# Kernel tuning notes

Hardware: AMD Instinct MI355X
Metric: run time of the kernel (lower is better)

## Reference

```python
import jax, jax.numpy as jnp
import numpy as np

NEG_BIG = -9e15  # matches torch's -9000000000000000.0 mask value
ALPHA = 0.2      # LeakyReLU negative slope


def setup_inputs() -> dict:
    key = jax.random.key(0)
    k1, k2, k3 = jax.random.split(key, 3)
    B, N, Fin, Fout = 8, 2048, 64, 64
    h = jax.random.normal(k1, (B, N, Fin), dtype=jnp.float32)
    adj = jax.random.randint(k2, (B, N, N), 0, 2, dtype=jnp.int32)
    kW, ka = jax.random.split(k3)
    # xavier_uniform with gain=1.414
    gW = 1.414 * np.sqrt(6.0 / (Fin + Fout))
    W = jax.random.uniform(kW, (Fin, Fout), minval=-gW, maxval=gW, dtype=jnp.float32)
    ga = 1.414 * np.sqrt(6.0 / (2 * Fout + 1))
    a = jax.random.uniform(ka, (2 * Fout, 1), minval=-ga, maxval=ga, dtype=jnp.float32)
    return {"h": h, "adj": adj, "W": W, "a": a}


def reference(h, adj, W, a):
    # Wh: [B, N, Fout]
    Wh = jnp.einsum("bnf,fo->bno", h, W)
    Fout = W.shape[1]
    a1 = a[:Fout, 0]   # source part of attention vector
    a2 = a[Fout:, 0]   # target part
    # e_ij = leakyrelu(a1.Wh_i + a2.Wh_j) -- rank-1 decomposition of the
    # repeat/cat construction; avoids the [B,N,N,2F] intermediate.
    s = Wh @ a1        # [B, N]
    t = Wh @ a2        # [B, N]
    e = s[:, :, None] + t[:, None, :]            # [B, N, N]
    e = jnp.where(e > 0, e, ALPHA * e)           # LeakyReLU
    e = jnp.where(adj > 0, e, NEG_BIG)           # adjacency mask
    attention = jax.nn.softmax(e, axis=2)
    # dropout omitted: reference is eval-mode (F.dropout is identity when not training)
    h_prime = jnp.einsum("bij,bjo->bio", attention, Wh)
    return jax.nn.elu(h_prime)                   # concat=True branch
```

## Files before the change

### kernel.cpp

```cpp
#include <hip/hip_runtime.h>


#define NB 8
#define NN 2048
#define NF 64
#define ALPHA 0.2f

typedef __attribute__((ext_vector_type(8))) short  short8;
typedef __attribute__((ext_vector_type(4))) float  f32x4;

static __device__ __forceinline__ unsigned short f2bf(float f) {
    unsigned u = __builtin_bit_cast(unsigned, f);
    u += 0x7fffu + ((u >> 16) & 1u);
    return (unsigned short)(u >> 16);
}

__global__ __launch_bounds__(256) void k1_wh_st(
    const float* __restrict__ h, const float* __restrict__ W,
    const float* __restrict__ a, unsigned short* __restrict__ whT,
    float* __restrict__ sw, float* __restrict__ tw)
{
    __shared__ float W_l[64 * 65];
    __shared__ float wa[128];
    __shared__ float tile[4 * 16 * 65];

    const int tid  = threadIdx.x;
    const int lane = tid & 63, wv = tid >> 6;
    const int im   = lane & 15, kq = lane >> 4;

    #pragma unroll
    for (int k = 0; k < 16; ++k) {
        int e = tid + 256 * k;
        W_l[(e >> 6) * 65 + (e & 63)] = W[e];
    }
    __syncthreads();

    if (tid < 128) {
        int f = tid & 63;
        const float* ap = a + (tid >> 6) * 64;
        float acc = 0.f;
        #pragma unroll 8
        for (int o = 0; o < 64; ++o) acc += W_l[f * 65 + o] * ap[o];
        wa[tid] = acc;
    }
    __syncthreads();

    short8 bf[4][2];
    #pragma unroll
    for (int nb = 0; nb < 4; ++nb)
        #pragma unroll
        for (int ks = 0; ks < 2; ++ks)
            #pragma unroll
            for (int u = 0; u < 8; ++u)
                bf[nb][ks][u] = (short)f2bf(W_l[(ks * 32 + kq * 8 + u) * 65 + nb * 16 + im]);

    const int row0 = blockIdx.x * 64 + wv * 16;
    const int bb = row0 >> 11, n_base = row0 & 2047;
    const float* hrow = h + (size_t)(row0 + im) * 64;

    float hv[2][8];
    short8 af[2];
    float sp = 0.f, tp = 0.f;
    #pragma unroll
    for (int ks = 0; ks < 2; ++ks) {
        float4 A = *(const float4*)(hrow + ks * 32 + kq * 8);
        float4 Bv = *(const float4*)(hrow + ks * 32 + kq * 8 + 4);
        hv[ks][0] = A.x;  hv[ks][1] = A.y;  hv[ks][2] = A.z;  hv[ks][3] = A.w;
        hv[ks][4] = Bv.x; hv[ks][5] = Bv.y; hv[ks][6] = Bv.z; hv[ks][7] = Bv.w;
        #pragma unroll
        for (int u = 0; u < 8; ++u) {
            int f = ks * 32 + kq * 8 + u;
            sp += hv[ks][u] * wa[f];
            tp += hv[ks][u] * wa[64 + f];
            af[ks][u] = (short)f2bf(hv[ks][u]);
        }
    }
    sp += __shfl_xor(sp, 16, 64); sp += __shfl_xor(sp, 32, 64);
    tp += __shfl_xor(tp, 16, 64); tp += __shfl_xor(tp, 32, 64);
    if (lane < 16) {
        sw[row0 + lane] = sp;
        tw[row0 + lane] = tp;
    }

    f32x4 acc[4] = {{0.f,0.f,0.f,0.f},{0.f,0.f,0.f,0.f},{0.f,0.f,0.f,0.f},{0.f,0.f,0.f,0.f}};
    #pragma unroll
    for (int ks = 0; ks < 2; ++ks)
        #pragma unroll
        for (int nb = 0; nb < 4; ++nb)
            acc[nb] = __builtin_amdgcn_mfma_f32_16x16x32_bf16(af[ks], bf[nb][ks], acc[nb], 0, 0, 0);

    #pragma unroll
    for (int nb = 0; nb < 4; ++nb)
        #pragma unroll
        for (int r = 0; r < 4; ++r)
            tile[wv * 1040 + (kq * 4 + r) * 65 + nb * 16 + im] = acc[nb][r];
    __syncthreads();

    #pragma unroll
    for (int k = 0; k < 16; ++k) {
        int o = kq + 4 * k;
        float v = tile[wv * 1040 + im * 65 + o];
        whT[(size_t)(bb * 64 + o) * 2048 + n_base + im] = f2bf(v);
    }
}

__global__ __launch_bounds__(256, 4) void k2_attn(
    const int* __restrict__ adj, const unsigned short* __restrict__ whT,
    const float* __restrict__ sw, const float* __restrict__ tw,
    float* __restrict__ out)
{
    __shared__ float cpart[4 * 1040];
    __shared__ float zp[64];

    const int tid  = threadIdx.x;
    const int lane = tid & 63, wv = tid >> 6;
    const int im   = lane & 15, kq = lane >> 4;
    const int b    = blockIdx.x >> 7;
    const int i0   = (blockIdx.x & 127) << 4;

    const int j00 = wv * 512 + kq * 8;
    const int*   adj_p = adj + ((size_t)(b * 2048 + i0 + im) * 2048 + j00);
    const float* t_p   = tw + (size_t)b * 2048 + j00;
    const unsigned short* whp0 = whT + ((size_t)(b * 64 +  0 + im) * 2048 + j00);
    const unsigned short* whp1 = whT + ((size_t)(b * 64 + 16 + im) * 2048 + j00);
    const unsigned short* whp2 = whT + ((size_t)(b * 64 + 32 + im) * 2048 + j00);
    const unsigned short* whp3 = whT + ((size_t)(b * 64 + 48 + im) * 2048 + j00);
    const float sl = sw[b * 2048 + i0 + im];

    f32x4 acc0 = {0.f,0.f,0.f,0.f}, acc1 = {0.f,0.f,0.f,0.f};
    f32x4 acc2 = {0.f,0.f,0.f,0.f}, acc3 = {0.f,0.f,0.f,0.f};
    float zs = 0.f;

    int4   ca = *(const int4*)(adj_p),     cb = *(const int4*)(adj_p + 4);
    float4 ta = *(const float4*)(t_p),     tb = *(const float4*)(t_p + 4);

    #pragma unroll 1
    for (int s = 0; s < 16; ++s) {
        short8 w0 = *(const short8*)(const void*)(whp0 + s * 32);
        short8 w1 = *(const short8*)(const void*)(whp1 + s * 32);
        short8 w2 = *(const short8*)(const void*)(whp2 + s * 32);
        short8 w3 = *(const short8*)(const void*)(whp3 + s * 32);

        int4 na = {0,0,0,0}, nb_ = {0,0,0,0};
        float4 nta = {0.f,0.f,0.f,0.f}, ntb = {0.f,0.f,0.f,0.f};
        if (s < 15) {
            na  = *(const int4*)(adj_p + (s + 1) * 32);
            nb_ = *(const int4*)(adj_p + (s + 1) * 32 + 4);
            nta = *(const float4*)(t_p + (s + 1) * 32);
            ntb = *(const float4*)(t_p + (s + 1) * 32 + 4);
        }

        short8 af;
        {
            float tv[8] = {ta.x, ta.y, ta.z, ta.w, tb.x, tb.y, tb.z, tb.w};
            int   av[8] = {ca.x, ca.y, ca.z, ca.w, cb.x, cb.y, cb.z, cb.w};
            #pragma unroll
            for (int u = 0; u < 8; ++u) {
                float e = sl + tv[u];
                e = e > 0.f ? e : ALPHA * e;
                float wgt = (av[u] > 0) ? __expf(e) : 0.f;
                zs += wgt;
                af[u] = (short)f2bf(wgt);
            }
        }

        acc0 = __builtin_amdgcn_mfma_f32_16x16x32_bf16(af, w0, acc0, 0, 0, 0);
        acc1 = __builtin_amdgcn_mfma_f32_16x16x32_bf16(af, w1, acc1, 0, 0, 0);
        acc2 = __builtin_amdgcn_mfma_f32_16x16x32_bf16(af, w2, acc2, 0, 0, 0);
        acc3 = __builtin_amdgcn_mfma_f32_16x16x32_bf16(af, w3, acc3, 0, 0, 0);

        ca = na; cb = nb_; ta = nta; tb = ntb;
    }

    zs += __shfl_xor(zs, 16, 64);
    zs += __shfl_xor(zs, 32, 64);
    if (lane < 16) zp[wv * 16 + lane] = zs;

    #pragma unroll
    for (int r = 0; r < 4; ++r) {
        cpart[wv * 1040 + (kq * 4 + r) * 65 +  0 + im] = acc0[r];
        cpart[wv * 1040 + (kq * 4 + r) * 65 + 16 + im] = acc1[r];
        cpart[wv * 1040 + (kq * 4 + r) * 65 + 32 + im] = acc2[r];
        cpart[wv * 1040 + (kq * 4 + r) * 65 + 48 + im] = acc3[r];
    }
    __syncthreads();

    #pragma unroll
    for (int k = 0; k < 4; ++k) {
        int idx = tid + 256 * k;
        int i = idx >> 6, o = idx & 63;
        float ssum = cpart[0 * 1040 + i * 65 + o] + cpart[1 * 1040 + i * 65 + o]
                   + cpart[2 * 1040 + i * 65 + o] + cpart[3 * 1040 + i * 65 + o];
        float z = zp[i] + zp[16 + i] + zp[32 + i] + zp[48 + i];
        if (z == 0.f) z = 1.f;
        float r = ssum / z;
        out[((size_t)(b * 2048 + i0 + i)) * 64 + o] = r > 0.f ? r : expm1f(r);
    }
}

extern "C" void kernel_launch(void* const* d_in, const int* in_sizes, int n_in,
                              void* d_out, int out_size, void* d_ws, size_t ws_size,
                              hipStream_t stream) {
    const float* h   = (const float*)d_in[0];
    const int*   adj = (const int*)d_in[1];
    const float* W   = (const float*)d_in[2];
    const float* a   = (const float*)d_in[3];
    float* out = (float*)d_out;

    unsigned short* whT = (unsigned short*)d_ws;
    float* sw = (float*)((char*)d_ws + 2097152);
    float* tw = (float*)((char*)d_ws + 2097152 + 65536);

    hipLaunchKernelGGL(k1_wh_st, dim3(256), dim3(256), 0, stream, h, W, a, whT, sw, tw);
    hipLaunchKernelGGL(k2_attn, dim3(1024), dim3(256), 0, stream, adj, whT, sw, tw, out);
}
```

Measured before the change: 226.7 us.

## Pre-pack adjacency into bitmask in first kernel; stage t vector in LDS

The first kernel gains extra blocks that read the int32 adjacency matrix and compress it into a 1-bit-per-entry mask. The attention kernel then reads the compact mask instead of the full int32 rows, and loads the per-batch t vector into shared memory. The main loop is fully unrolled, prefetches the Wh tiles, and uses a cheaper bf16 pack through perm. The adjacency still has to be read once, and writing plus re-reading the mask adds traffic. Since each adjacency row was only read once before, the gain depends mostly on the leaner inner loop and better load overlap.

```diff
diff --git a/kernel.cpp b/kernel.cpp
--- a/kernel.cpp
+++ b/kernel.cpp
@@ -1,9 +1,6 @@
 #include <hip/hip_runtime.h>
 
 
-#define NB 8
-#define NN 2048
-#define NF 64
 #define ALPHA 0.2f
 
 typedef __attribute__((ext_vector_type(8))) short  short8;
@@ -15,16 +12,47 @@
     return (unsigned short)(u >> 16);
 }
 
-__global__ __launch_bounds__(256) void k1_wh_st(
-    const float* __restrict__ h, const float* __restrict__ W,
-    const float* __restrict__ a, unsigned short* __restrict__ whT,
-    float* __restrict__ sw, float* __restrict__ tw)
+static __device__ __forceinline__ unsigned pack_bf2(float lo, float hi) {
+    unsigned ulo = __builtin_bit_cast(unsigned, lo) + 0x8000u;
+    unsigned uhi = __builtin_bit_cast(unsigned, hi) + 0x8000u;
+    return __builtin_amdgcn_perm(uhi, ulo, 0x07060302);
+}
+
+__global__ __launch_bounds__(256) void k01(
+    const float* __restrict__ h, const int* __restrict__ adj,
+    const float* __restrict__ W, const float* __restrict__ a,
+    unsigned short* __restrict__ whT, float* __restrict__ sw,
+    float* __restrict__ tw, unsigned* __restrict__ mask)
 {
     __shared__ float W_l[64 * 65];
     __shared__ float wa[128];
     __shared__ float tile[4 * 16 * 65];
 
-    const int tid  = threadIdx.x;
+    const int tid = threadIdx.x;
+
+    if (blockIdx.x >= 256) {
+        const int mb = blockIdx.x - 256;
+        const int4* a4 = (const int4*)adj;
+        #pragma unroll 1
+        for (int batch = 0; batch < 4; ++batch) {
+            const size_t base = (size_t)mb * 8192 + batch * 2048 + tid;
+            int4 v[8];
+            #pragma unroll
+            for (int it = 0; it < 8; ++it) v[it] = a4[base + it * 256];
+            #pragma unroll
+            for (int it = 0; it < 8; ++it) {
+                unsigned nib = (v[it].x != 0 ? 1u : 0u) | (v[it].y != 0 ? 2u : 0u)
+                             | (v[it].z != 0 ? 4u : 0u) | (v[it].w != 0 ? 8u : 0u);
+                unsigned w = nib << ((tid & 7) * 4);
+                w |= __shfl_xor(w, 1, 64);
+                w |= __shfl_xor(w, 2, 64);
+                w |= __shfl_xor(w, 4, 64);
+                if ((tid & 7) == 0) mask[(base + it * 256) >> 3] = w;
+            }
+        }
+        return;
+    }
+
     const int lane = tid & 63, wv = tid >> 6;
     const int im   = lane & 15, kq = lane >> 4;
 
@@ -105,10 +133,11 @@
 }
 
 __global__ __launch_bounds__(256, 4) void k2_attn(
-    const int* __restrict__ adj, const unsigned short* __restrict__ whT,
+    const unsigned* __restrict__ mask, const unsigned short* __restrict__ whT,
     const float* __restrict__ sw, const float* __restrict__ tw,
     float* __restrict__ out)
 {
+    __shared__ float t_l[2048];
     __shared__ float cpart[4 * 1040];
     __shared__ float zp[64];
 
@@ -118,58 +147,75 @@
     const int b    = blockIdx.x >> 7;
     const int i0   = (blockIdx.x & 127) << 4;
 
+    {
+        const float4* tp4 = (const float4*)(tw + (size_t)b * 2048);
+        *(float4*)&t_l[tid * 4]         = tp4[tid];
+        *(float4*)&t_l[(tid + 256) * 4] = tp4[tid + 256];
+    }
+
+    const unsigned* mrow = mask + (size_t)(b * 2048 + i0 + im) * 64 + wv * 16;
+    uint4 m0 = *(const uint4*)mrow,        m1 = *(const uint4*)(mrow + 4);
+    uint4 m2 = *(const uint4*)(mrow + 8),  m3 = *(const uint4*)(mrow + 12);
+    unsigned mm[16] = {m0.x, m0.y, m0.z, m0.w, m1.x, m1.y, m1.z, m1.w,
+                       m2.x, m2.y, m2.z, m2.w, m3.x, m3.y, m3.z, m3.w};
+
+    const float sl = sw[b * 2048 + i0 + im];
     const int j00 = wv * 512 + kq * 8;
-    const int*   adj_p = adj + ((size_t)(b * 2048 + i0 + im) * 2048 + j00);
-    const float* t_p   = tw + (size_t)b * 2048 + j00;
     const unsigned short* whp0 = whT + ((size_t)(b * 64 +  0 + im) * 2048 + j00);
     const unsigned short* whp1 = whT + ((size_t)(b * 64 + 16 + im) * 2048 + j00);
     const unsigned short* whp2 = whT + ((size_t)(b * 64 + 32 + im) * 2048 + j00);
     const unsigned short* whp3 = whT + ((size_t)(b * 64 + 48 + im) * 2048 + j00);
-    const float sl = sw[b * 2048 + i0 + im];
+    const int tbase = wv * 512 + kq * 8;
+
+    __syncthreads();
 
     f32x4 acc0 = {0.f,0.f,0.f,0.f}, acc1 = {0.f,0.f,0.f,0.f};
     f32x4 acc2 = {0.f,0.f,0.f,0.f}, acc3 = {0.f,0.f,0.f,0.f};
     float zs = 0.f;
 
-    int4   ca = *(const int4*)(adj_p),     cb = *(const int4*)(adj_p + 4);
-    float4 ta = *(const float4*)(t_p),     tb = *(const float4*)(t_p + 4);
-
-    #pragma unroll 1
+    short8 w0 = *(const short8*)(const void*)whp0;
+    short8 w1 = *(const short8*)(const void*)whp1;
+    short8 w2 = *(const short8*)(const void*)whp2;
+    short8 w3 = *(const short8*)(const void*)whp3;
+
+    #pragma unroll
     for (int s = 0; s < 16; ++s) {
-        short8 w0 = *(const short8*)(const void*)(whp0 + s * 32);
-        short8 w1 = *(const short8*)(const void*)(whp1 + s * 32);
-        short8 w2 = *(const short8*)(const void*)(whp2 + s * 32);
-        short8 w3 = *(const short8*)(const void*)(whp3 + s * 32);
-
-        int4 na = {0,0,0,0}, nb_ = {0,0,0,0};
-        float4 nta = {0.f,0.f,0.f,0.f}, ntb = {0.f,0.f,0.f,0.f};
+        short8 n0 = w0, n1 = w1, n2 = w2, n3 = w3;
         if (s < 15) {
-            na  = *(const int4*)(adj_p + (s + 1) * 32);
-            nb_ = *(const int4*)(adj_p + (s + 1) * 32 + 4);
-            nta = *(const float4*)(t_p + (s + 1) * 32);
-            ntb = *(const float4*)(t_p + (s + 1) * 32 + 4);
-        }
-
-        short8 af;
-        {
-            float tv[8] = {ta.x, ta.y, ta.z, ta.w, tb.x, tb.y, tb.z, tb.w};
-            int   av[8] = {ca.x, ca.y, ca.z, ca.w, cb.x, cb.y, cb.z, cb.w};
-            #pragma unroll
-            for (int u = 0; u < 8; ++u) {
-                float e = sl + tv[u];
-                e = e > 0.f ? e : ALPHA * e;
-                float wgt = (av[u] > 0) ? __expf(e) : 0.f;
-                zs += wgt;
-                af[u] = (short)f2bf(wgt);
-            }
-        }
+            n0 = *(const short8*)(const void*)(whp0 + (s + 1) * 32);
+            n1 = *(const short8*)(const void*)(whp1 + (s + 1) * 32);
+            n2 = *(const short8*)(const void*)(whp2 + (s + 1) * 32);
+            n3 = *(const short8*)(const void*)(whp3 + (s + 1) * 32);
+        }
+
+        float4 tA = *(const float4*)&t_l[tbase + s * 32];
+        float4 tB = *(const float4*)&t_l[tbase + s * 32 + 4];
+        const unsigned mbyte = (mm[s] >> (kq * 8)) & 0xffu;
+
+        float tv[8] = {tA.x, tA.y, tA.z, tA.w, tB.x, tB.y, tB.z, tB.w};
+        float p[8];
+        #pragma unroll
+        for (int u = 0; u < 8; ++u) {
+            float e = sl + tv[u];
+            e = fmaxf(e, ALPHA * e);
+            float w = __expf(e);
+            p[u] = (mbyte & (1u << u)) ? w : 0.f;
+            zs += p[u];
+        }
+
+        int4 ai;
+        ai.x = (int)pack_bf2(p[0], p[1]);
+        ai.y = (int)pack_bf2(p[2], p[3]);
+        ai.z = (int)pack_bf2(p[4], p[5]);
+        ai.w = (int)pack_bf2(p[6], p[7]);
+        short8 af = __builtin_bit_cast(short8, ai);
 
         acc0 = __builtin_amdgcn_mfma_f32_16x16x32_bf16(af, w0, acc0, 0, 0, 0);
         acc1 = __builtin_amdgcn_mfma_f32_16x16x32_bf16(af, w1, acc1, 0, 0, 0);
         acc2 = __builtin_amdgcn_mfma_f32_16x16x32_bf16(af, w2, acc2, 0, 0, 0);
         acc3 = __builtin_amdgcn_mfma_f32_16x16x32_bf16(af, w3, acc3, 0, 0, 0);
 
-        ca = na; cb = nb_; ta = nta; tb = ntb;
+        w0 = n0; w1 = n1; w2 = n2; w3 = n3;
     }
 
     zs += __shfl_xor(zs, 16, 64);
@@ -208,9 +254,10 @@
     float* out = (float*)d_out;
 
     unsigned short* whT = (unsigned short*)d_ws;
-    float* sw = (float*)((char*)d_ws + 2097152);
-    float* tw = (float*)((char*)d_ws + 2097152 + 65536);
-
-    hipLaunchKernelGGL(k1_wh_st, dim3(256), dim3(256), 0, stream, h, W, a, whT, sw, tw);
-    hipLaunchKernelGGL(k2_attn, dim3(1024), dim3(256), 0, stream, adj, whT, sw, tw, out);
-}
+    float* sw  = (float*)((char*)d_ws + 2097152);
+    float* tw  = (float*)((char*)d_ws + 2097152 + 65536);
+    unsigned* mask = (unsigned*)((char*)d_ws + 2097152 + 131072);
+
+    hipLaunchKernelGGL(k01, dim3(1280), dim3(256), 0, stream, h, adj, W, a, whT, sw, tw, mask);
+    hipLaunchKernelGGL(k2_attn, dim3(1024), dim3(256), 0, stream, mask, whT, sw, tw, out);
+}
```

Result: slower. 236.1 us (+4.2%).
